# Performance work log

Hardware: AMD Instinct MI355X
Metric: run time of the kernel (lower is better)

The kernel has to match this reference:

```python
import jax, jax.numpy as jnp
import numpy as np

N = 50000        # nodes
E = 800000       # edges (before self-loops)
F_IN = 128       # in_features
HID = 128        # hidden_size
HEADS = 4
NEG_SLOPE = 0.2  # PyG GATConv default


def setup_inputs() -> dict:
    key = jax.random.key(0)
    ks = jax.random.split(key, 16)
    def w(k, shape, fan_in):
        return jax.random.normal(k, shape, dtype=jnp.float32) / np.sqrt(fan_in)
    x = jax.random.normal(ks[0], (N, F_IN), dtype=jnp.float32)
    edge_index = jax.random.randint(ks[1], (2, E), 0, N, dtype=jnp.int64)
    return {
        "x": x,
        "edge_index": edge_index,
        # encoder: HEADS independent GATConv(F_IN -> HID, heads=1)
        "enc_W": w(ks[2], (HEADS, F_IN, HID), F_IN),
        "enc_asrc": w(ks[3], (HEADS, HID), HID),
        "enc_adst": w(ks[4], (HEADS, HID), HID),
        "enc_b": jnp.zeros((HEADS, HID), jnp.float32),
        "enc_lin_W": w(ks[5], (HEADS * HID, HID), HEADS * HID),
        "enc_lin_b": jnp.zeros((HID,), jnp.float32),
        # decoder: HEADS independent GATConv(HID -> F_IN, heads=1)
        "dec_W": w(ks[6], (HEADS, HID, F_IN), HID),
        "dec_asrc": w(ks[7], (HEADS, F_IN), F_IN),
        "dec_adst": w(ks[8], (HEADS, F_IN), F_IN),
        "dec_b": jnp.zeros((HEADS, F_IN), jnp.float32),
        "dec_lin_W": w(ks[9], (HEADS * F_IN, F_IN), HEADS * F_IN),
        "dec_lin_b": jnp.zeros((F_IN,), jnp.float32),
    }


def _gat_head(x, src, dst, W, a_src, a_dst, b, n):
    # PyG GATConv, heads=1: h = xW; e = leaky_relu(a_src.h_src + a_dst.h_dst)
    # alpha = segment-softmax over incoming edges of dst; out = scatter-add + b
    h = x @ W                                   # [n, out]
    e = (h @ a_src)[src] + (h @ a_dst)[dst]     # [Etot]
    e = jax.nn.leaky_relu(e, NEG_SLOPE)
    m = jax.ops.segment_max(e, dst, num_segments=n)
    ew = jnp.exp(e - m[dst])
    denom = jax.ops.segment_sum(ew, dst, num_segments=n)
    alpha = ew / denom[dst]                     # self-loops guarantee denom > 0
    out = jax.ops.segment_sum(alpha[:, None] * h[src], dst, num_segments=n)
    return out + b


def _multihead(x, src, dst, Ws, asrc, adst, bs, lin_W, lin_b, n):
    heads = [_gat_head(x, src, dst, Ws[h], asrc[h], adst[h], bs[h], n)
             for h in range(Ws.shape[0])]
    cat = jnp.concatenate(heads, axis=1)        # [n, heads*out]
    return jax.nn.relu(cat @ lin_W + lin_b)


def reference(x, edge_index, enc_W, enc_asrc, enc_adst, enc_b, enc_lin_W,
              enc_lin_b, dec_W, dec_asrc, dec_adst, dec_b, dec_lin_W,
              dec_lin_b):
    n = x.shape[0]
    loop = jnp.arange(n, dtype=edge_index.dtype)
    src = jnp.concatenate([edge_index[0], loop])  # add self-loops (PyG default)
    dst = jnp.concatenate([edge_index[1], loop])
    enc = _multihead(x, src, dst, enc_W, enc_asrc, enc_adst, enc_b,
                     enc_lin_W, enc_lin_b, n)
    dec = _multihead(enc, src, dst, dec_W, dec_asrc, dec_adst, dec_b,
                     dec_lin_W, dec_lin_b, n)
    return dec
```

## Files before the change

kernel.cpp:

```cpp
#include <hip/hip_runtime.h>
#include <hip/hip_fp16.h>
#include <cstdint>
#include <cstddef>


#define FDIM   128
#define HEADS  4
#define HCAT   512

typedef unsigned short u16;
typedef __attribute__((ext_vector_type(4))) float f32x4;
typedef __attribute__((ext_vector_type(8))) _Float16 f16x8;

__device__ __forceinline__ u16 f2h_bits(float f) {
    _Float16 h = (_Float16)f;
    return *(u16*)&h;
}

__global__ void k_detect(const void* ei, int E, int N, int* flag) {
    if (threadIdx.x == 0 && blockIdx.x == 0) {
        const long long* p = (const long long*)ei;
        int bad = 0;
        int n = E < 64 ? E : 64;
        for (int i = 0; i < n; ++i) {
            long long v = p[i];
            if (v < 0 || v >= (long long)N) bad = 1;
        }
        *flag = bad;
    }
}

__device__ __forceinline__ int edge_at(const void* ei, int is32, long long pos) {
    return is32 ? ((const int*)ei)[pos] : (int)(((const long long*)ei)[pos]);
}

__global__ void k_zero_i32(int* p, int n) {
    int i = blockIdx.x * blockDim.x + threadIdx.x;
    if (i < n) p[i] = 0;
}

__global__ void k_count(const void* ei, const int* flag, int E, int N, int* deg) {
    int e = blockIdx.x * blockDim.x + threadIdx.x;
    int Etot = E + N;
    if (e >= Etot) return;
    int is32 = *flag;
    int dst = (e < E) ? edge_at(ei, is32, (long long)E + e) : (e - E);
    atomicAdd(&deg[dst], 1);
}

#define SCAN_BLOCKS 256
#define SCAN_TPB    256

__global__ __launch_bounds__(SCAN_TPB) void k_scan1(const int* __restrict__ deg,
                                                    int* __restrict__ bsum, int N) {
    __shared__ int sdata[SCAN_TPB];
    int b = blockIdx.x;
    int chunk = (N + SCAN_BLOCKS - 1) / SCAN_BLOCKS;
    int start = b * chunk;
    int end = start + chunk;
    if (start > N) start = N;
    if (end > N) end = N;
    int s = 0;
    for (int i = start + threadIdx.x; i < end; i += SCAN_TPB) s += deg[i];
    sdata[threadIdx.x] = s;
    __syncthreads();
    for (int o = SCAN_TPB / 2; o; o >>= 1) {
        if (threadIdx.x < o) sdata[threadIdx.x] += sdata[threadIdx.x + o];
        __syncthreads();
    }
    if (threadIdx.x == 0) bsum[b] = sdata[0];
}

__global__ __launch_bounds__(SCAN_BLOCKS) void k_scan2(const int* __restrict__ bsum,
                                                       int* __restrict__ bbase,
                                                       int* __restrict__ off_last) {
    __shared__ int sdata[SCAN_BLOCKS];
    int t = threadIdx.x;
    sdata[t] = bsum[t];
    __syncthreads();
    for (int o = 1; o < SCAN_BLOCKS; o <<= 1) {
        int v = (t >= o) ? sdata[t - o] : 0;
        __syncthreads();
        sdata[t] += v;
        __syncthreads();
    }
    bbase[t] = (t == 0) ? 0 : sdata[t - 1];
    if (t == SCAN_BLOCKS - 1) *off_last = sdata[t];
}

__global__ __launch_bounds__(SCAN_TPB) void k_scan3(const int* __restrict__ deg,
                                                    const int* __restrict__ bbase,
                                                    int* __restrict__ off,
                                                    int* __restrict__ cur, int N) {
    __shared__ int sdata[SCAN_TPB];
    int b = blockIdx.x;
    int chunk = (N + SCAN_BLOCKS - 1) / SCAN_BLOCKS;
    int start = b * chunk;
    int end = start + chunk;
    if (start > N) start = N;
    if (end > N) end = N;
    int base = bbase[b];
    for (int i0 = start; i0 < end; i0 += SCAN_TPB) {
        int i = i0 + threadIdx.x;
        int v = (i < end) ? deg[i] : 0;
        sdata[threadIdx.x] = v;
        __syncthreads();
        for (int o = 1; o < SCAN_TPB; o <<= 1) {
            int u = (threadIdx.x >= o) ? sdata[threadIdx.x - o] : 0;
            __syncthreads();
            sdata[threadIdx.x] += u;
            __syncthreads();
        }
        if (i < end) {
            int excl = base + sdata[threadIdx.x] - v;
            off[i] = excl;
            cur[i] = excl;
        }
        base += sdata[SCAN_TPB - 1];
        __syncthreads();
    }
}

__global__ void k_fill(const void* ei, const int* flag, int E, int N, int* cur, int* csr) {
    int e = blockIdx.x * blockDim.x + threadIdx.x;
    int Etot = E + N;
    if (e >= Etot) return;
    int is32 = *flag;
    int src, dst;
    if (e < E) {
        src = edge_at(ei, is32, e);
        dst = edge_at(ei, is32, (long long)E + e);
    } else {
        src = e - E;
        dst = e - E;
    }
    int pos = atomicAdd(&cur[dst], 1);
    csr[pos] = src;
}

__global__ void k_splitw(const float* __restrict__ W, u16* __restrict__ hi,
                         u16* __restrict__ lo, int nblk, int K) {
    int idx = blockIdx.x * blockDim.x + threadIdx.x;
    int total = nblk * K * 128;
    if (idx >= total) return;
    int blk = idx / (K * 128);
    int rem = idx - blk * K * 128;
    int k = rem >> 7, col = rem & 127;
    float v = W[idx];
    _Float16 hh = (_Float16)v;
    _Float16 ll = (_Float16)(v - (float)hh);
    size_t o = (size_t)blk * 128 * K + (size_t)col * K + k;
    hi[o] = *(u16*)&hh;
    lo[o] = *(u16*)&ll;
}

__global__ void k_cvt_f16(const float* __restrict__ X, u16* __restrict__ out, int n) {
    int i = blockIdx.x * blockDim.x + threadIdx.x;
    if (i >= n) return;
    out[i] = f2h_bits(X[i]);
}

template <int MODE>
__global__ __launch_bounds__(256) void k_gemm_f16(
    const u16* __restrict__ A, int lda,
    const u16* __restrict__ Bthi, const u16* __restrict__ Btlo,
    const float* __restrict__ bias,
    const float* __restrict__ asrc, const float* __restrict__ adst,
    float* __restrict__ C, u16* __restrict__ Cb1,
    float* __restrict__ ssrc, float* __restrict__ sdst,
    int ldc, int M, int K)
{
    __shared__ alignas(16) char smem[24576];
    __shared__ float sred[512];
    const int ASH = 0, BHI = 8192, BLO = 16384;
    int tid = threadIdx.x;
    int bm0 = blockIdx.x * 128;
    int yb = blockIdx.y;

    int wid = tid >> 6, lane = tid & 63;
    int wr = wid >> 1, wc = wid & 1;
    int fr = lane & 15, g = lane >> 4;

    f32x4 acc[4][4] = {};

    int arow = tid >> 1, ahalf = tid & 1;
    bool ain = (bm0 + arow) < M;
    const u16* aptr = A + (size_t)(bm0 + arow) * lda + ahalf * 16;
    int bcol = tid & 127, bhalf = tid >> 7;
    const u16* bph = Bthi + (size_t)yb * 128 * K + (size_t)bcol * K + bhalf * 16;
    const u16* bpl = Btlo + (size_t)yb * 128 * K + (size_t)bcol * K + bhalf * 16;

    int abase = arow * 64 + ahalf * 32;
    int asw = (arow & 7) << 4;
    int bbase = bcol * 64 + bhalf * 32;
    int bsw = (bcol & 7) << 4;

    uint4 va0, va1, vb0, vb1, vm0, vm1;
    if (ain) { va0 = *(const uint4*)(aptr); va1 = *(const uint4*)(aptr + 8); }
    else { va0 = make_uint4(0, 0, 0, 0); va1 = make_uint4(0, 0, 0, 0); }
    vb0 = *(const uint4*)(bph);
    vb1 = *(const uint4*)(bph + 8);
    vm0 = *(const uint4*)(bpl);
    vm1 = *(const uint4*)(bpl + 8);

    for (int k0 = 0; k0 < K; k0 += 32) {
        *(uint4*)(smem + ASH + ((abase +  0) ^ asw)) = va0;
        *(uint4*)(smem + ASH + ((abase + 16) ^ asw)) = va1;
        *(uint4*)(smem + BHI + ((bbase +  0) ^ bsw)) = vb0;
        *(uint4*)(smem + BHI + ((bbase + 16) ^ bsw)) = vb1;
        *(uint4*)(smem + BLO + ((bbase +  0) ^ bsw)) = vm0;
        *(uint4*)(smem + BLO + ((bbase + 16) ^ bsw)) = vm1;

        __syncthreads();

        if (k0 + 32 < K) {
            int kn = k0 + 32;
            if (ain) { va0 = *(const uint4*)(aptr + kn); va1 = *(const uint4*)(aptr + kn + 8); }
            else { va0 = make_uint4(0, 0, 0, 0); va1 = make_uint4(0, 0, 0, 0); }
            vb0 = *(const uint4*)(bph + kn);
            vb1 = *(const uint4*)(bph + kn + 8);
            vm0 = *(const uint4*)(bpl + kn);
            vm1 = *(const uint4*)(bpl + kn + 8);
        }

        f16x8 af[4], bh[4], bl[4];
#pragma unroll
        for (int mi = 0; mi < 4; ++mi) {
            int r = wr * 64 + mi * 16 + fr;
            int off = (r * 64 + g * 16) ^ ((r & 7) << 4);
            af[mi] = *(f16x8*)(smem + ASH + off);
        }
#pragma unroll
        for (int nj = 0; nj < 4; ++nj) {
            int c = wc * 64 + nj * 16 + fr;
            int off = (c * 64 + g * 16) ^ ((c & 7) << 4);
            bh[nj] = *(f16x8*)(smem + BHI + off);
            bl[nj] = *(f16x8*)(smem + BLO + off);
        }

#pragma unroll
        for (int mi = 0; mi < 4; ++mi)
#pragma unroll
            for (int nj = 0; nj < 4; ++nj) {
                acc[mi][nj] = __builtin_amdgcn_mfma_f32_16x16x32_f16(af[mi], bh[nj], acc[mi][nj], 0, 0, 0);
                acc[mi][nj] = __builtin_amdgcn_mfma_f32_16x16x32_f16(af[mi], bl[nj], acc[mi][nj], 0, 0, 0);
            }
        __syncthreads();
    }

#pragma unroll
    for (int mi = 0; mi < 4; ++mi) {
#pragma unroll
        for (int q = 0; q < 4; ++q) {
            int r = bm0 + wr * 64 + mi * 16 + g * 4 + q;
            if (r >= M) continue;
#pragma unroll
            for (int nj = 0; nj < 4; ++nj) {
                int c = wc * 64 + nj * 16 + fr;
                float v = acc[mi][nj][q];
                if (MODE == 0) {
                    Cb1[(size_t)r * ldc + yb * 128 + c] = f2h_bits(v);
                } else if (MODE == 1) {
                    v += bias[c];
                    v = fmaxf(v, 0.f);
                    Cb1[(size_t)r * ldc + c] = f2h_bits(v);
                } else {
                    v += bias[c];
                    v = fmaxf(v, 0.f);
                    C[(size_t)r * ldc + c] = v;
                }
            }
        }
    }

    if (MODE == 0) {
        float asv[4], adv[4];
        const float* app = asrc + yb * FDIM;
        const float* dpp = adst + yb * FDIM;
#pragma unroll
        for (int nj = 0; nj < 4; ++nj) {
            int c = wc * 64 + nj * 16 + fr;
            asv[nj] = app[c];
            adv[nj] = dpp[c];
        }
#pragma unroll
        for (int mi = 0; mi < 4; ++mi) {
#pragma unroll
            for (int q = 0; q < 4; ++q) {
                float ps = 0.f, pd = 0.f;
#pragma unroll
                for (int nj = 0; nj < 4; ++nj) {
                    ps += acc[mi][nj][q] * asv[nj];
                    pd += acc[mi][nj][q] * adv[nj];
                }
#pragma unroll
                for (int o = 1; o < 16; o <<= 1) {
                    ps += __shfl_xor(ps, o);
                    pd += __shfl_xor(pd, o);
                }
                if (fr == 0) {
                    int row128 = wr * 64 + mi * 16 + g * 4 + q;
                    sred[(row128 * 2 + wc) * 2 + 0] = ps;
                    sred[(row128 * 2 + wc) * 2 + 1] = pd;
                }
            }
        }
        __syncthreads();
        {
            int rg = tid >> 1;
            int which = tid & 1;
            int r = bm0 + rg;
            if (r < M) {
                float v = sred[(rg * 2 + 0) * 2 + which] + sred[(rg * 2 + 1) * 2 + which];
                float* dstp = which ? sdst : ssrc;
                dstp[(size_t)yb * M + r] = v;
            }
        }
    }
}

__global__ __launch_bounds__(64) void k_aggregate(
    const u16* __restrict__ Hb, const int* __restrict__ off,
    const int* __restrict__ csr, const float* __restrict__ ssrc,
    const float* __restrict__ sdst, const float* __restrict__ bvec,
    u16* __restrict__ Gh, int N) {
    int n = blockIdx.x;
    int lane = threadIdx.x;
    int o0 = __builtin_amdgcn_readfirstlane(off[n]);
    int o1 = __builtin_amdgcn_readfirstlane(off[n + 1]);
    int h = lane >> 4;
    int col0 = lane * 8;
    float sdh = sdst[(size_t)h * N + n];
    const float* ssrc_h = ssrc + (size_t)h * N;
    float denom = 0.f;
    float acc[8] = {0.f, 0.f, 0.f, 0.f, 0.f, 0.f, 0.f, 0.f};

    auto body = [&](float ew, uint4 hv) {
        const __half2* hp = (const __half2*)&hv;
#pragma unroll
        for (int j = 0; j < 4; ++j) {
            float2 f = __half22float2(hp[j]);
            acc[2 * j]     += ew * f.x;
            acc[2 * j + 1] += ew * f.y;
        }
    };

    int i = o0;
    for (; i + 4 <= o1; i += 4) {
        int s0 = csr[i + 0], s1 = csr[i + 1], s2 = csr[i + 2], s3 = csr[i + 3];
        uint4 v0 = *(const uint4*)&Hb[(size_t)s0 * HCAT + col0];
        uint4 v1 = *(const uint4*)&Hb[(size_t)s1 * HCAT + col0];
        uint4 v2 = *(const uint4*)&Hb[(size_t)s2 * HCAT + col0];
        uint4 v3 = *(const uint4*)&Hb[(size_t)s3 * HCAT + col0];
        float e0 = ssrc_h[s0] + sdh, e1 = ssrc_h[s1] + sdh;
        float e2 = ssrc_h[s2] + sdh, e3 = ssrc_h[s3] + sdh;
        e0 = e0 >= 0.f ? e0 : 0.2f * e0;
        e1 = e1 >= 0.f ? e1 : 0.2f * e1;
        e2 = e2 >= 0.f ? e2 : 0.2f * e2;
        e3 = e3 >= 0.f ? e3 : 0.2f * e3;
        float w0 = __expf(e0), w1 = __expf(e1), w2 = __expf(e2), w3 = __expf(e3);
        denom += (w0 + w1) + (w2 + w3);
        body(w0, v0);
        body(w1, v1);
        body(w2, v2);
        body(w3, v3);
    }
    for (; i < o1; ++i) {
        int s = csr[i];
        uint4 v = *(const uint4*)&Hb[(size_t)s * HCAT + col0];
        float e = ssrc_h[s] + sdh;
        e = e >= 0.f ? e : 0.2f * e;
        float ew = __expf(e);
        denom += ew;
        body(ew, v);
    }

    float inv = 1.f / denom;
    u16 hs[8];
#pragma unroll
    for (int k = 0; k < 8; ++k) {
        int col = col0 + k;
        float v = acc[k] * inv + bvec[h * FDIM + (col & 127)];
        hs[k] = f2h_bits(v);
    }
    *(uint4*)&Gh[(size_t)n * HCAT + col0] = *(uint4*)hs;
}

extern "C" void kernel_launch(void* const* d_in, const int* in_sizes, int n_in,
                              void* d_out, int out_size, void* d_ws, size_t ws_size,
                              hipStream_t stream) {
    const float* x = (const float*)d_in[0];
    const void* ei = d_in[1];
    const float* encW = (const float*)d_in[2];
    const float* enc_asrc = (const float*)d_in[3];
    const float* enc_adst = (const float*)d_in[4];
    const float* enc_b = (const float*)d_in[5];
    const float* enc_linW = (const float*)d_in[6];
    const float* enc_linb = (const float*)d_in[7];
    const float* decW = (const float*)d_in[8];
    const float* dec_asrc = (const float*)d_in[9];
    const float* dec_adst = (const float*)d_in[10];
    const float* dec_b = (const float*)d_in[11];
    const float* dec_linW = (const float*)d_in[12];
    const float* dec_linb = (const float*)d_in[13];

    int N = in_sizes[0] / FDIM;
    int E = in_sizes[1] / 2;
    int Etot = E + N;

    char* w = (char*)d_ws;
    size_t o = 0;
    auto alloc = [&](size_t bytes) -> char* {
        char* p = w + o;
        o += (bytes + 255) & ~(size_t)255;
        return p;
    };
    int* flag = (int*)alloc(4);
    int* deg = (int*)alloc((size_t)N * 4);
    int* off = (int*)alloc((size_t)(N + 1) * 4);
    int* cur = (int*)alloc((size_t)N * 4);
    int* csr = (int*)alloc((size_t)Etot * 4);
    int* bsum = (int*)alloc(SCAN_BLOCKS * 4);
    int* bbase = (int*)alloc(SCAN_BLOCKS * 4);
    float* ssrc = (float*)alloc((size_t)HEADS * N * 4);
    float* sdst = (float*)alloc((size_t)HEADS * N * 4);
    u16* Gh = (u16*)alloc((size_t)N * HCAT * 2);
    u16* Hb = (u16*)alloc((size_t)N * HCAT * 2);
    u16* xh = (u16*)alloc((size_t)N * FDIM * 2);
    u16* X2h = (u16*)alloc((size_t)N * FDIM * 2);
    u16* encWt_h = (u16*)alloc((size_t)HEADS * FDIM * FDIM * 2);
    u16* encWt_l = (u16*)alloc((size_t)HEADS * FDIM * FDIM * 2);
    u16* linWt_h = (u16*)alloc((size_t)HCAT * FDIM * 2);
    u16* linWt_l = (u16*)alloc((size_t)HCAT * FDIM * 2);
    u16* decWt_h = (u16*)alloc((size_t)HEADS * FDIM * FDIM * 2);
    u16* decWt_l = (u16*)alloc((size_t)HEADS * FDIM * FDIM * 2);
    u16* dlinWt_h = (u16*)alloc((size_t)HCAT * FDIM * 2);
    u16* dlinWt_l = (u16*)alloc((size_t)HCAT * FDIM * 2);
    (void)ws_size;

    k_detect<<<1, 64, 0, stream>>>(ei, E, N, flag);
    k_zero_i32<<<(N + 255) / 256, 256, 0, stream>>>(deg, N);
    k_count<<<(Etot + 255) / 256, 256, 0, stream>>>(ei, flag, E, N, deg);
    k_scan1<<<SCAN_BLOCKS, SCAN_TPB, 0, stream>>>(deg, bsum, N);
    k_scan2<<<1, SCAN_BLOCKS, 0, stream>>>(bsum, bbase, off + N);
    k_scan3<<<SCAN_BLOCKS, SCAN_TPB, 0, stream>>>(deg, bbase, off, cur, N);
    k_fill<<<(Etot + 255) / 256, 256, 0, stream>>>(ei, flag, E, N, cur, csr);

    int wtot = HEADS * FDIM * FDIM;
    k_splitw<<<(wtot + 255) / 256, 256, 0, stream>>>(encW, encWt_h, encWt_l, HEADS, FDIM);
    k_splitw<<<(wtot + 255) / 256, 256, 0, stream>>>(enc_linW, linWt_h, linWt_l, 1, HCAT);
    k_splitw<<<(wtot + 255) / 256, 256, 0, stream>>>(decW, decWt_h, decWt_l, HEADS, FDIM);
    k_splitw<<<(wtot + 255) / 256, 256, 0, stream>>>(dec_linW, dlinWt_h, dlinWt_l, 1, HCAT);
    k_cvt_f16<<<(N * FDIM + 255) / 256, 256, 0, stream>>>(x, xh, N * FDIM);

    int mblocks = (N + 127) / 128;

    k_gemm_f16<0><<<dim3(mblocks, 4), 256, 0, stream>>>(
        xh, FDIM, encWt_h, encWt_l, nullptr, enc_asrc, enc_adst,
        nullptr, Hb, ssrc, sdst, HCAT, N, FDIM);
    k_aggregate<<<N, 64, 0, stream>>>(Hb, off, csr, ssrc, sdst, enc_b, Gh, N);
    k_gemm_f16<1><<<dim3(mblocks, 1), 256, 0, stream>>>(
        Gh, HCAT, linWt_h, linWt_l, enc_linb, nullptr, nullptr,
        nullptr, X2h, nullptr, nullptr, FDIM, N, HCAT);

    k_gemm_f16<0><<<dim3(mblocks, 4), 256, 0, stream>>>(
        X2h, FDIM, decWt_h, decWt_l, nullptr, dec_asrc, dec_adst,
        nullptr, Hb, ssrc, sdst, HCAT, N, FDIM);
    k_aggregate<<<N, 64, 0, stream>>>(Hb, off, csr, ssrc, sdst, dec_b, Gh, N);
    k_gemm_f16<2><<<dim3(mblocks, 1), 256, 0, stream>>>(
        Gh, HCAT, dlinWt_h, dlinWt_l, dec_linb, nullptr, nullptr,
        (float*)d_out, nullptr, nullptr, nullptr, FDIM, N, HCAT);
}
```

Before: 532.5 us.

## Split GAT aggregation into edge-weight pass and column-slab gather kernel

Computes per-edge softmax weights and per-node denominators in a separate kernel that stores weight/source pairs per head. The aggregation then runs eight column slabs per node, with each lane gathering one half-precision element per edge. This is meant to increase parallelism and avoid recomputing exponentials across lanes. In exchange it adds a large intermediate edge buffer, an extra launch, and many narrow 2-byte gathers instead of 16-byte vector loads.

Result: slower. 682.2 us (+28.1%).

```diff
diff --git a/kernel.cpp b/kernel.cpp
--- a/kernel.cpp
+++ b/kernel.cpp
@@ -15,6 +15,10 @@
 __device__ __forceinline__ u16 f2h_bits(float f) {
     _Float16 h = (_Float16)f;
     return *(u16*)&h;
+}
+__device__ __forceinline__ float h2f_bits(u16 b) {
+    _Float16 h = *(_Float16*)&b;
+    return (float)h;
 }
 
 __global__ void k_detect(const void* ei, int E, int N, int* flag) {
@@ -319,71 +323,71 @@
     }
 }
 
-__global__ __launch_bounds__(64) void k_aggregate(
-    const u16* __restrict__ Hb, const int* __restrict__ off,
-    const int* __restrict__ csr, const float* __restrict__ ssrc,
-    const float* __restrict__ sdst, const float* __restrict__ bvec,
-    u16* __restrict__ Gh, int N) {
+__global__ __launch_bounds__(64) void k_alpha(
+    const int* __restrict__ off, const int* __restrict__ csr,
+    const float* __restrict__ ssrc, const float* __restrict__ sdst,
+    uint2* __restrict__ edata, float* __restrict__ denom, int N, int Etot) {
     int n = blockIdx.x;
     int lane = threadIdx.x;
+    int o0 = off[n], o1 = off[n + 1];
+    float sd[4];
+#pragma unroll
+    for (int h = 0; h < HEADS; ++h) sd[h] = sdst[(size_t)h * N + n];
+    float dsum[4] = {0.f, 0.f, 0.f, 0.f};
+    for (int i = o0 + lane; i < o1; i += 64) {
+        int s = csr[i];
+#pragma unroll
+        for (int h = 0; h < HEADS; ++h) {
+            float e = ssrc[(size_t)h * N + s] + sd[h];
+            e = e >= 0.f ? e : 0.2f * e;
+            float wgt = __expf(e);
+            dsum[h] += wgt;
+            edata[(size_t)h * Etot + i] = make_uint2(__float_as_uint(wgt), (unsigned)s);
+        }
+    }
+#pragma unroll
+    for (int h = 0; h < HEADS; ++h)
+        for (int o = 32; o; o >>= 1) dsum[h] += __shfl_xor(dsum[h], o);
+    if (lane == 0) {
+#pragma unroll
+        for (int h = 0; h < HEADS; ++h) denom[(size_t)h * N + n] = dsum[h];
+    }
+}
+
+__global__ __launch_bounds__(256) void k_agg_slab(
+    const u16* __restrict__ Hb, const int* __restrict__ off,
+    const uint2* __restrict__ edata, const float* __restrict__ denom,
+    const float* __restrict__ bvec, u16* __restrict__ Gh, int N, int Etot) {
+    int bid = blockIdx.x;
+    int slab = bid & 7;
+    int n = (bid >> 3) * 4 + (threadIdx.x >> 6);
+    if (n >= N) return;
+    int lane = threadIdx.x & 63;
+    int h = slab >> 1;
+    int col = slab * 64 + lane;
+    const uint2* ed = edata + (size_t)h * Etot;
     int o0 = __builtin_amdgcn_readfirstlane(off[n]);
     int o1 = __builtin_amdgcn_readfirstlane(off[n + 1]);
-    int h = lane >> 4;
-    int col0 = lane * 8;
-    float sdh = sdst[(size_t)h * N + n];
-    const float* ssrc_h = ssrc + (size_t)h * N;
-    float denom = 0.f;
-    float acc[8] = {0.f, 0.f, 0.f, 0.f, 0.f, 0.f, 0.f, 0.f};
-
-    auto body = [&](float ew, uint4 hv) {
-        const __half2* hp = (const __half2*)&hv;
-#pragma unroll
-        for (int j = 0; j < 4; ++j) {
-            float2 f = __half22float2(hp[j]);
-            acc[2 * j]     += ew * f.x;
-            acc[2 * j + 1] += ew * f.y;
-        }
-    };
-
+    float acc = 0.f;
     int i = o0;
     for (; i + 4 <= o1; i += 4) {
-        int s0 = csr[i + 0], s1 = csr[i + 1], s2 = csr[i + 2], s3 = csr[i + 3];
-        uint4 v0 = *(const uint4*)&Hb[(size_t)s0 * HCAT + col0];
-        uint4 v1 = *(const uint4*)&Hb[(size_t)s1 * HCAT + col0];
-        uint4 v2 = *(const uint4*)&Hb[(size_t)s2 * HCAT + col0];
-        uint4 v3 = *(const uint4*)&Hb[(size_t)s3 * HCAT + col0];
-        float e0 = ssrc_h[s0] + sdh, e1 = ssrc_h[s1] + sdh;
-        float e2 = ssrc_h[s2] + sdh, e3 = ssrc_h[s3] + sdh;
-        e0 = e0 >= 0.f ? e0 : 0.2f * e0;
-        e1 = e1 >= 0.f ? e1 : 0.2f * e1;
-        e2 = e2 >= 0.f ? e2 : 0.2f * e2;
-        e3 = e3 >= 0.f ? e3 : 0.2f * e3;
-        float w0 = __expf(e0), w1 = __expf(e1), w2 = __expf(e2), w3 = __expf(e3);
-        denom += (w0 + w1) + (w2 + w3);
-        body(w0, v0);
-        body(w1, v1);
-        body(w2, v2);
-        body(w3, v3);
+        uint2 e0 = ed[i + 0], e1 = ed[i + 1], e2 = ed[i + 2], e3 = ed[i + 3];
+        u16 g0 = Hb[(size_t)e0.y * HCAT + col];
+        u16 g1 = Hb[(size_t)e1.y * HCAT + col];
+        u16 g2 = Hb[(size_t)e2.y * HCAT + col];
+        u16 g3 = Hb[(size_t)e3.y * HCAT + col];
+        acc += __uint_as_float(e0.x) * h2f_bits(g0);
+        acc += __uint_as_float(e1.x) * h2f_bits(g1);
+        acc += __uint_as_float(e2.x) * h2f_bits(g2);
+        acc += __uint_as_float(e3.x) * h2f_bits(g3);
     }
     for (; i < o1; ++i) {
-        int s = csr[i];
-        uint4 v = *(const uint4*)&Hb[(size_t)s * HCAT + col0];
-        float e = ssrc_h[s] + sdh;
-        e = e >= 0.f ? e : 0.2f * e;
-        float ew = __expf(e);
-        denom += ew;
-        body(ew, v);
-    }
-
-    float inv = 1.f / denom;
-    u16 hs[8];
-#pragma unroll
-    for (int k = 0; k < 8; ++k) {
-        int col = col0 + k;
-        float v = acc[k] * inv + bvec[h * FDIM + (col & 127)];
-        hs[k] = f2h_bits(v);
-    }
-    *(uint4*)&Gh[(size_t)n * HCAT + col0] = *(uint4*)hs;
+        uint2 e = ed[i];
+        acc += __uint_as_float(e.x) * h2f_bits(Hb[(size_t)e.y * HCAT + col]);
+    }
+    float inv = 1.f / denom[(size_t)h * N + n];
+    float v = acc * inv + bvec[h * FDIM + (slab & 1) * 64 + lane];
+    Gh[(size_t)n * HCAT + col] = f2h_bits(v);
 }
 
 extern "C" void kernel_launch(void* const* d_in, const int* in_sizes, int n_in,
@@ -424,6 +428,8 @@
     int* bbase = (int*)alloc(SCAN_BLOCKS * 4);
     float* ssrc = (float*)alloc((size_t)HEADS * N * 4);
     float* sdst = (float*)alloc((size_t)HEADS * N * 4);
+    float* denom = (float*)alloc((size_t)HEADS * N * 4);
+    uint2* edata = (uint2*)alloc((size_t)HEADS * Etot * 8);
     u16* Gh = (u16*)alloc((size_t)N * HCAT * 2);
     u16* Hb = (u16*)alloc((size_t)N * HCAT * 2);
     u16* xh = (u16*)alloc((size_t)N * FDIM * 2);
@@ -454,11 +460,13 @@
     k_cvt_f16<<<(N * FDIM + 255) / 256, 256, 0, stream>>>(x, xh, N * FDIM);
 
     int mblocks = (N + 127) / 128;
+    int aggblocks = ((N + 3) / 4) * 8;
 
     k_gemm_f16<0><<<dim3(mblocks, 4), 256, 0, stream>>>(
         xh, FDIM, encWt_h, encWt_l, nullptr, enc_asrc, enc_adst,
         nullptr, Hb, ssrc, sdst, HCAT, N, FDIM);
-    k_aggregate<<<N, 64, 0, stream>>>(Hb, off, csr, ssrc, sdst, enc_b, Gh, N);
+    k_alpha<<<N, 64, 0, stream>>>(off, csr, ssrc, sdst, edata, denom, N, Etot);
+    k_agg_slab<<<aggblocks, 256, 0, stream>>>(Hb, off, edata, denom, enc_b, Gh, N, Etot);
     k_gemm_f16<1><<<dim3(mblocks, 1), 256, 0, stream>>>(
         Gh, HCAT, linWt_h, linWt_l, enc_linb, nullptr, nullptr,
         nullptr, X2h, nullptr, nullptr, FDIM, N, HCAT);
@@ -466,7 +474,8 @@
     k_gemm_f16<0><<<dim3(mblocks, 4), 256, 0, stream>>>(
         X2h, FDIM, decWt_h, decWt_l, nullptr, dec_asrc, dec_adst,
         nullptr, Hb, ssrc, sdst, HCAT, N, FDIM);
-    k_aggregate<<<N, 64, 0, stream>>>(Hb, off, csr, ssrc, sdst, dec_b, Gh, N);
+    k_alpha<<<N, 64, 0, stream>>>(off, csr, ssrc, sdst, edata, denom, N, Etot);
+    k_agg_slab<<<aggblocks, 256, 0, stream>>>(Hb, off, edata, denom, dec_b, Gh, N, Etot);
     k_gemm_f16<2><<<dim3(mblocks, 1), 256, 0, stream>>>(
         Gh, HCAT, dlinWt_h, dlinWt_l, dec_linb, nullptr, nullptr,
         (float*)d_out, nullptr, nullptr, nullptr, FDIM, N, HCAT);
```
